# Performance work log

Measured on AMD Instinct MI355X. Metric: run time of the kernel, lower is better.

## Reference

```python
import jax, jax.numpy as jnp
import numpy as np
from jax import lax


def setup_inputs() -> dict:
    key = jax.random.key(0)
    k1, k2 = jax.random.split(key)
    B, T, D, O = 8, 8192, 512, 512
    x = jax.random.normal(k1, (B, T, D), dtype=jnp.float32)
    # Dense kernel over concat([h_t, state]) -> width 2*D
    W = jax.random.normal(k2, (2 * D, O), dtype=jnp.float32) * (1.0 / np.sqrt(2 * D))
    b = jnp.zeros((O,), dtype=jnp.float32)
    decay = jnp.float32(0.95)
    return {"x": x, "W": W, "b": b, "decay": decay}


def reference(x, W, b, decay):
    # x: [B, T, D]; W: [2D, O]; b: [O]; decay: scalar lambda
    B, T, D = x.shape
    lam = jnp.clip(decay, 0.5, 0.999)  # keras constraint on the decay weight
    h_avg = jnp.mean(x, axis=0)  # [T, D] batch-mean per timestep

    # EMA recurrence: s_t = lam * s_{t-1} + (1 - lam) * h_avg_t, s_{-1} = 0
    def step(s, a):
        s = lam * s + (1.0 - lam) * a
        return s, s

    _, states = lax.scan(step, jnp.zeros((D,), x.dtype), h_avg)  # [T, D]

    # proj(concat([h_t, s_t])) = h_t @ W_h + s_t @ W_s + b (fused, no concat materialized)
    W_h, W_s = W[:D], W[D:]
    out = jnp.einsum('btd,do->bto', x, W_h) + jnp.einsum('td,do->to', states, W_s)[None] + b
    return out  # [B, T, O]
```

## Files before the change

### kernel.cpp

```cpp
#include <hip/hip_runtime.h>
#include <hip/hip_bf16.h>
#include <stdint.h>

#define T_DIM 8192
#define B_DIM 8
#define D_DIM 512
#define O_DIM 512

typedef __attribute__((ext_vector_type(4))) float f32x4;
typedef __attribute__((ext_vector_type(8))) short short8;
typedef __attribute__((ext_vector_type(4))) unsigned short us4;
typedef __attribute__((ext_vector_type(4))) uint32_t u32x4;

__device__ __forceinline__ unsigned short f2bf(float f) {
  union { float f; uint32_t u; } v; v.f = f;
  uint32_t u = v.u + 0x7FFFu + ((v.u >> 16) & 1u);
  return (unsigned short)(u >> 16);
}

__device__ __forceinline__ uint32_t cvtpk(float a, float b) {
  uint32_t r;
  asm("v_cvt_pk_bf16_f32 %0, %1, %2" : "=v"(r) : "v"(a), "v"(b));
  return r;
}

__device__ __forceinline__ void gload_lds16(const void* g, void* l) {
  __builtin_amdgcn_global_load_lds(
      (const __attribute__((address_space(1))) void*)g,
      (__attribute__((address_space(3))) void*)l, 16, 0, 0);
}

__device__ __forceinline__ float clip_lam(const float* decay) {
  return fminf(fmaxf(decay[0], 0.5f), 0.999f);
}

__global__ void mean_kernel(const float* __restrict__ x, float* __restrict__ havg) {
  int idx = blockIdx.x * 256 + threadIdx.x;
  const f32x4* x4 = (const f32x4*)x;
  const size_t stride = (size_t)T_DIM * D_DIM / 4;
  f32x4 v[8];
#pragma unroll
  for (int b = 0; b < B_DIM; ++b) v[b] = x4[(size_t)b * stride + idx];
  f32x4 s = ((v[0] + v[1]) + (v[2] + v[3])) + ((v[4] + v[5]) + (v[6] + v[7]));
  s *= 0.125f;
  ((f32x4*)havg)[idx] = s;
}

__global__ void wconv_kernel(const float* __restrict__ W, unsigned short* __restrict__ Wt) {
  __shared__ float tile[64][65];
  int bk = blockIdx.x >> 3;
  int bn = blockIdx.x & 7;
  int tr = threadIdx.x >> 4;
  int tc = threadIdx.x & 15;
#pragma unroll
  for (int i = 0; i < 4; ++i) {
    int row = i * 16 + tr;
    f32x4 v = *(const f32x4*)&W[(size_t)(bk * 64 + row) * O_DIM + bn * 64 + tc * 4];
#pragma unroll
    for (int j = 0; j < 4; ++j) tile[row][tc * 4 + j] = v[j];
  }
  __syncthreads();
#pragma unroll
  for (int i = 0; i < 4; ++i) {
    int nl = i * 16 + tr;
    us4 o;
#pragma unroll
    for (int j = 0; j < 4; ++j) o[j] = f2bf(tile[tc * 4 + j][nl]);
    int kg = bk * 64 + tc * 4;
    int h = kg >> 9;
    int k = kg & 511;
    *(us4*)&Wt[(size_t)h * (512 * 512) + (size_t)(bn * 64 + nl) * 512 + k] = o;
  }
}

#define CHUNK 128
#define NCHUNK (T_DIM / CHUNK)

__global__ void scanA_kernel(float* __restrict__ havg, const float* __restrict__ decay) {
  int chunk = blockIdx.x >> 1;
  int d = ((blockIdx.x & 1) << 8) + threadIdx.x;
  float lam = clip_lam(decay);
  float om = 1.0f - lam;
  size_t base = (size_t)chunk * CHUNK * D_DIM + d;
  float cur[16], nxt[16];
#pragma unroll
  for (int i = 0; i < 16; ++i) cur[i] = havg[base + (size_t)i * D_DIM];
  float s = 0.f;
  for (int blk = 0; blk < 8; ++blk) {
    if (blk < 7) {
#pragma unroll
      for (int i = 0; i < 16; ++i)
        nxt[i] = havg[base + (size_t)((blk + 1) * 16 + i) * D_DIM];
    }
#pragma unroll
    for (int i = 0; i < 16; ++i) {
      s = lam * s + om * cur[i];
      havg[base + (size_t)(blk * 16 + i) * D_DIM] = s;
    }
#pragma unroll
    for (int i = 0; i < 16; ++i) cur[i] = nxt[i];
  }
}

__global__ void scanB_kernel(const float* __restrict__ havg, const float* __restrict__ decay,
                             float* __restrict__ carry) {
  int d = blockIdx.x * 256 + threadIdx.x;
  float lam = clip_lam(decay);
  float l2 = lam * lam;
  float l4 = l2 * l2;
  float l8 = l4 * l4;
  float l16 = l8 * l8;
  float l32 = l16 * l16;
  float l64 = l32 * l32;
  float l128 = l64 * l64;
  float e[NCHUNK];
#pragma unroll
  for (int c = 0; c < NCHUNK; ++c)
    e[c] = havg[((size_t)c * CHUNK + CHUNK - 1) * D_DIM + d];
  float s = 0.f;
#pragma unroll
  for (int c = 0; c < NCHUNK; ++c) {
    s = l128 * s + e[c];
    carry[c * D_DIM + d] = s;
  }
}

__global__ void scanC_kernel(const float* __restrict__ havg, const float* __restrict__ carry,
                             const float* __restrict__ decay, unsigned short* __restrict__ st) {
  int idx = blockIdx.x * 256 + threadIdx.x;
  int t = idx >> 7;
  int d4 = idx & 127;
  int c = t >> 7;
  int k = t & 127;
  float lam = clip_lam(decay);
  float w = exp2f((float)(k + 1) * __log2f(lam));
  f32x4 p = ((const f32x4*)havg)[idx];
  f32x4 cin = {0.f, 0.f, 0.f, 0.f};
  if (c > 0) cin = ((const f32x4*)carry)[(size_t)(c - 1) * 128 + d4];
  us4 o;
#pragma unroll
  for (int j = 0; j < 4; ++j) o[j] = f2bf(p[j] + w * cin[j]);
  ((us4*)st)[idx] = o;
}

__global__ __launch_bounds__(256, 4)
void gemm128bf(const unsigned short* __restrict__ A, const unsigned short* __restrict__ Bt,
               const float* __restrict__ extra, float* __restrict__ C) {
  __shared__ __align__(16) char smem[2][16384];

  int nwg = gridDim.x;
  int bid = blockIdx.x;
  int swz = (bid & 7) * (nwg >> 3) + (bid >> 3);
  int tm = swz >> 2, tn = swz & 3;
  int brow = tm << 7, bcol = tn << 7;

  int tid = threadIdx.x;
  int wave = tid >> 6, lane = tid & 63;
  int wr = (wave >> 1) << 6, wc = (wave & 1) << 6;
  const int lr = lane & 15, lkb = lane >> 4;

  const int soct = ((lane & 3) ^ ((lane >> 3) & 3)) << 3;
  const int pm = (lr >> 1) & 3;

  const size_t a_base = (size_t)(brow + (wave << 4) + (lane >> 2)) * 512 + soct;
  const size_t b_base = (size_t)(bcol + (wave << 4) + (lane >> 2)) * 512 + soct;

  f32x4 acc[4][4];
#pragma unroll
  for (int m = 0; m < 4; ++m)
#pragma unroll
    for (int n = 0; n < 4; ++n) acc[m][n] = (f32x4){0.f, 0.f, 0.f, 0.f};

#define STAGE(buf, kt_)                                                        \
  {                                                                            \
    int k0_ = (kt_) << 5;                                                      \
    _Pragma("unroll")                                                          \
    for (int it = 0; it < 2; ++it)                                             \
      gload_lds16(A + a_base + (size_t)(it << 15) + k0_,                       \
                  &smem[buf][(((it << 2) + wave) << 10)]);                     \
    _Pragma("unroll")                                                          \
    for (int it = 0; it < 2; ++it)                                             \
      gload_lds16(Bt + b_base + (size_t)(it << 15) + k0_,                      \
                  &smem[buf][8192 + (((it << 2) + wave) << 10)]);              \
  }

  STAGE(0, 0);

#pragma unroll 2
  for (int kt = 0; kt < 16; ++kt) {
    const int cur = kt & 1;
    if (kt < 15) {
      STAGE(cur ^ 1, kt + 1);
      asm volatile("s_waitcnt vmcnt(4)" ::: "memory");
    } else {
      asm volatile("s_waitcnt vmcnt(0)" ::: "memory");
    }
    __builtin_amdgcn_s_barrier();
    __builtin_amdgcn_sched_barrier(0);

    const unsigned short* As = (const unsigned short*)&smem[cur][0];
    const unsigned short* Bs = (const unsigned short*)&smem[cur][8192];
    short8 af[4], bfr[4];
#pragma unroll
    for (int m = 0; m < 4; ++m)
      af[m] = *(const short8*)(As + (size_t)(wr + (m << 4) + lr) * 32 + ((lkb ^ pm) << 3));
#pragma unroll
    for (int n = 0; n < 4; ++n)
      bfr[n] = *(const short8*)(Bs + (size_t)(wc + (n << 4) + lr) * 32 + ((lkb ^ pm) << 3));

#pragma unroll
    for (int m = 0; m < 4; ++m)
#pragma unroll
      for (int n = 0; n < 4; ++n)
        acc[m][n] = __builtin_amdgcn_mfma_f32_16x16x32_bf16(af[m], bfr[n], acc[m][n], 0, 0, 0);

    __builtin_amdgcn_sched_barrier(0);
    __builtin_amdgcn_s_barrier();
  }
#undef STAGE

  float* tp = (float*)&smem[0][0] + (size_t)wave * 2048;
#pragma unroll
  for (int m = 0; m < 4; ++m) {
#pragma unroll
    for (int n = 0; n < 4; ++n)
#pragma unroll
      for (int j = 0; j < 4; ++j)
        tp[((lkb << 2) + j) * 68 + (n << 4) + lr] = acc[m][n][j];
    __syncthreads();
#pragma unroll
    for (int p = 0; p < 4; ++p) {
      int rl = (p << 2) + (lane >> 4);
      int c0 = (lane & 15) << 2;
      f32x4 v = *(const f32x4*)(tp + rl * 68 + c0);
      int row = brow + wr + (m << 4) + rl;
      int col = bcol + wc + c0;
      f32x4 e = *(const f32x4*)&extra[col];
      v += e;
      *(f32x4*)&C[(size_t)row * O_DIM + col] = v;
    }
    __syncthreads();
  }
}

__global__ __launch_bounds__(256, 4)
void gemm128xf(const float* __restrict__ X, const unsigned short* __restrict__ Bt,
               const float* __restrict__ extra, float* __restrict__ C) {
  __shared__ __align__(16) char smem[2][16384];

  int nwg = gridDim.x;
  int bid = blockIdx.x;
  int swz = (bid & 7) * (nwg >> 3) + (bid >> 3);
  int tm = swz >> 2, tn = swz & 3;
  int brow = tm << 7, bcol = tn << 7;

  int tid = threadIdx.x;
  int wave = tid >> 6, lane = tid & 63;
  int wr = (wave >> 1) << 6, wc = (wave & 1) << 6;
  const int lr = lane & 15, lkb = lane >> 4;
  const int pm = (lr >> 1) & 3;

  const int arow = tid >> 1, ahalf = tid & 1;
  const float* agp = X + (size_t)(brow + arow) * 512 + (ahalf << 4);
  const int aperm = (arow >> 1) & 3;
  const int aw0 = arow * 64 + (((ahalf << 1) ^ aperm) << 4);
  const int aw1 = aw0 ^ 16;

  const int soct = ((lane & 3) ^ ((lane >> 3) & 3)) << 3;
  const size_t b_base = (size_t)(bcol + (wave << 4) + (lane >> 2)) * 512 + soct;

  f32x4 acc[4][4];
#pragma unroll
  for (int m = 0; m < 4; ++m)
#pragma unroll
    for (int n = 0; n < 4; ++n) acc[m][n] = (f32x4){0.f, 0.f, 0.f, 0.f};

  f32x4 a0, a1, a2, a3;
#define ALOAD(kt_)                                                             \
  {                                                                            \
    const float* p_ = agp + ((kt_) << 5);                                      \
    a0 = *(const f32x4*)p_;       a1 = *(const f32x4*)(p_ + 4);                \
    a2 = *(const f32x4*)(p_ + 8); a3 = *(const f32x4*)(p_ + 12);               \
  }
#define BSTAGE(buf, kt_)                                                       \
  {                                                                            \
    int k0_ = (kt_) << 5;                                                      \
    _Pragma("unroll")                                                          \
    for (int it = 0; it < 2; ++it)                                             \
      gload_lds16(Bt + b_base + (size_t)(it << 15) + k0_,                      \
                  &smem[buf][8192 + (((it << 2) + wave) << 10)]);              \
  }
#define AWRITE(buf)                                                            \
  {                                                                            \
    u32x4 w0_ = {cvtpk(a0[0], a0[1]), cvtpk(a0[2], a0[3]),                     \
                 cvtpk(a1[0], a1[1]), cvtpk(a1[2], a1[3])};                    \
    u32x4 w1_ = {cvtpk(a2[0], a2[1]), cvtpk(a2[2], a2[3]),                     \
                 cvtpk(a3[0], a3[1]), cvtpk(a3[2], a3[3])};                    \
    *(u32x4*)&smem[buf][aw0] = w0_;                                            \
    *(u32x4*)&smem[buf][aw1] = w1_;                                            \
  }

  ALOAD(0); BSTAGE(0, 0);
  AWRITE(0);
  __syncthreads();

#pragma unroll 2
  for (int kt = 0; kt < 16; ++kt) {
    const int cur = kt & 1;
    if (kt < 15) { ALOAD(kt + 1); BSTAGE(cur ^ 1, kt + 1); }
    __builtin_amdgcn_sched_barrier(0);

    const unsigned short* As = (const unsigned short*)&smem[cur][0];
    const unsigned short* Bs = (const unsigned short*)&smem[cur][8192];
    short8 af[4], bfr[4];
#pragma unroll
    for (int m = 0; m < 4; ++m)
      af[m] = *(const short8*)(As + (size_t)(wr + (m << 4) + lr) * 32 + ((lkb ^ pm) << 3));
#pragma unroll
    for (int n = 0; n < 4; ++n)
      bfr[n] = *(const short8*)(Bs + (size_t)(wc + (n << 4) + lr) * 32 + ((lkb ^ pm) << 3));

#pragma unroll
    for (int m = 0; m < 4; ++m)
#pragma unroll
      for (int n = 0; n < 4; ++n)
        acc[m][n] = __builtin_amdgcn_mfma_f32_16x16x32_bf16(af[m], bfr[n], acc[m][n], 0, 0, 0);

    if (kt < 15) AWRITE(cur ^ 1);
    __syncthreads();
  }
#undef ALOAD
#undef BSTAGE
#undef AWRITE

  float* tp = (float*)&smem[0][0] + (size_t)wave * 2048;
#pragma unroll
  for (int m = 0; m < 4; ++m) {
#pragma unroll
    for (int n = 0; n < 4; ++n)
#pragma unroll
      for (int j = 0; j < 4; ++j)
        tp[((lkb << 2) + j) * 68 + (n << 4) + lr] = acc[m][n][j];
    __syncthreads();
#pragma unroll
    for (int p = 0; p < 4; ++p) {
      int rl = (p << 2) + (lane >> 4);
      int c0 = (lane & 15) << 2;
      f32x4 v = *(const f32x4*)(tp + rl * 68 + c0);
      int row = brow + wr + (m << 4) + rl;
      int col = bcol + wc + c0;
      f32x4 e = *(const f32x4*)&extra[(size_t)(row & (T_DIM - 1)) * O_DIM + col];
      v += e;
      *(f32x4*)&C[(size_t)row * O_DIM + col] = v;
    }
    __syncthreads();
  }
}

extern "C" void kernel_launch(void* const* d_in, const int* in_sizes, int n_in,
                              void* d_out, int out_size, void* d_ws, size_t ws_size,
                              hipStream_t stream) {
  (void)in_sizes; (void)n_in; (void)out_size; (void)ws_size;
  const float* x     = (const float*)d_in[0];
  const float* W     = (const float*)d_in[1];
  const float* bias  = (const float*)d_in[2];
  const float* decay = (const float*)d_in[3];
  float* out = (float*)d_out;

  char* ws = (char*)d_ws;
  size_t off = 0;
  float*          havg  = (float*)(ws + off);          off += 16777216;
  unsigned short* st    = (unsigned short*)(ws + off); off += 8388608;
  unsigned short* Wt    = (unsigned short*)(ws + off); off += 1048576;
  float*          sbar  = (float*)(ws + off);          off += 16777216;
  float*          carry = (float*)(ws + off);          off += 131072;

  mean_kernel<<<T_DIM * D_DIM / 4 / 256, 256, 0, stream>>>(x, havg);
  wconv_kernel<<<128, 256, 0, stream>>>(W, Wt);
  scanA_kernel<<<NCHUNK * 2, 256, 0, stream>>>(havg, decay);
  scanB_kernel<<<2, 256, 0, stream>>>(havg, decay, carry);
  scanC_kernel<<<T_DIM * D_DIM / 4 / 256, 256, 0, stream>>>(havg, carry, decay, st);
  gemm128bf<<<(T_DIM / 128) * 4, 256, 0, stream>>>(st, Wt + 512 * 512, bias, sbar);
  gemm128xf<<<(B_DIM * T_DIM / 128) * 4, 256, 0, stream>>>(x, Wt, sbar, out);
}
```

Before: 129.8 us.

## Load GEMM operands directly from global into MFMA registers, bypassing LDS staging

New measurement: 239.0 us. 84.1% more time.

```diff
diff --git a/kernel.cpp b/kernel.cpp
--- a/kernel.cpp
+++ b/kernel.cpp
@@ -243,10 +243,10 @@
   }
 }
 
-__global__ __launch_bounds__(256, 4)
-void gemm128xf(const float* __restrict__ X, const unsigned short* __restrict__ Bt,
-               const float* __restrict__ extra, float* __restrict__ C) {
-  __shared__ __align__(16) char smem[2][16384];
+__global__ __launch_bounds__(256, 3)
+void gemm_direct(const float* __restrict__ X, const unsigned short* __restrict__ Wt,
+                 const float* __restrict__ sbar, float* __restrict__ C) {
+  __shared__ __align__(16) char smem[32768];
 
   int nwg = gridDim.x;
   int bid = blockIdx.x;
@@ -258,16 +258,15 @@
   int wave = tid >> 6, lane = tid & 63;
   int wr = (wave >> 1) << 6, wc = (wave & 1) << 6;
   const int lr = lane & 15, lkb = lane >> 4;
-  const int pm = (lr >> 1) & 3;
-
-  const int arow = tid >> 1, ahalf = tid & 1;
-  const float* agp = X + (size_t)(brow + arow) * 512 + (ahalf << 4);
-  const int aperm = (arow >> 1) & 3;
-  const int aw0 = arow * 64 + (((ahalf << 1) ^ aperm) << 4);
-  const int aw1 = aw0 ^ 16;
-
-  const int soct = ((lane & 3) ^ ((lane >> 3) & 3)) << 3;
-  const size_t b_base = (size_t)(bcol + (wave << 4) + (lane >> 2)) * 512 + soct;
+
+  const float* ax[4];
+  const unsigned short* bw[4];
+#pragma unroll
+  for (int m = 0; m < 4; ++m)
+    ax[m] = X + (size_t)(brow + wr + (m << 4) + lr) * 512 + (lkb << 3);
+#pragma unroll
+  for (int n = 0; n < 4; ++n)
+    bw[n] = Wt + (size_t)(bcol + wc + (n << 4) + lr) * 512 + (lkb << 3);
 
   f32x4 acc[4][4];
 #pragma unroll
@@ -275,65 +274,48 @@
 #pragma unroll
     for (int n = 0; n < 4; ++n) acc[m][n] = (f32x4){0.f, 0.f, 0.f, 0.f};
 
-  f32x4 a0, a1, a2, a3;
-#define ALOAD(kt_)                                                             \
-  {                                                                            \
-    const float* p_ = agp + ((kt_) << 5);                                      \
-    a0 = *(const f32x4*)p_;       a1 = *(const f32x4*)(p_ + 4);                \
-    a2 = *(const f32x4*)(p_ + 8); a3 = *(const f32x4*)(p_ + 12);               \
-  }
-#define BSTAGE(buf, kt_)                                                       \
-  {                                                                            \
-    int k0_ = (kt_) << 5;                                                      \
-    _Pragma("unroll")                                                          \
-    for (int it = 0; it < 2; ++it)                                             \
-      gload_lds16(Bt + b_base + (size_t)(it << 15) + k0_,                      \
-                  &smem[buf][8192 + (((it << 2) + wave) << 10)]);              \
-  }
-#define AWRITE(buf)                                                            \
-  {                                                                            \
-    u32x4 w0_ = {cvtpk(a0[0], a0[1]), cvtpk(a0[2], a0[3]),                     \
-                 cvtpk(a1[0], a1[1]), cvtpk(a1[2], a1[3])};                    \
-    u32x4 w1_ = {cvtpk(a2[0], a2[1]), cvtpk(a2[2], a2[3]),                     \
-                 cvtpk(a3[0], a3[1]), cvtpk(a3[2], a3[3])};                    \
-    *(u32x4*)&smem[buf][aw0] = w0_;                                            \
-    *(u32x4*)&smem[buf][aw1] = w1_;                                            \
-  }
-
-  ALOAD(0); BSTAGE(0, 0);
-  AWRITE(0);
-  __syncthreads();
-
-#pragma unroll 2
+  f32x4 a0[4], a1[4];
+  short8 bl[4];
+#pragma unroll
+  for (int m = 0; m < 4; ++m) {
+    a0[m] = *(const f32x4*)(ax[m]);
+    a1[m] = *(const f32x4*)(ax[m] + 4);
+  }
+#pragma unroll
+  for (int n = 0; n < 4; ++n) bl[n] = *(const short8*)(bw[n]);
+
   for (int kt = 0; kt < 16; ++kt) {
-    const int cur = kt & 1;
-    if (kt < 15) { ALOAD(kt + 1); BSTAGE(cur ^ 1, kt + 1); }
-    __builtin_amdgcn_sched_barrier(0);
-
-    const unsigned short* As = (const unsigned short*)&smem[cur][0];
-    const unsigned short* Bs = (const unsigned short*)&smem[cur][8192];
-    short8 af[4], bfr[4];
+    short8 af[4];
+#pragma unroll
+    for (int m = 0; m < 4; ++m) {
+      union { short8 s; u32x4 u; } t;
+      t.u = (u32x4){cvtpk(a0[m][0], a0[m][1]), cvtpk(a0[m][2], a0[m][3]),
+                    cvtpk(a1[m][0], a1[m][1]), cvtpk(a1[m][2], a1[m][3])};
+      af[m] = t.s;
+    }
+    short8 bf[4];
+#pragma unroll
+    for (int n = 0; n < 4; ++n) bf[n] = bl[n];
+
+    if (kt < 15) {
+      int off = (kt + 1) << 5;
+#pragma unroll
+      for (int m = 0; m < 4; ++m) {
+        a0[m] = *(const f32x4*)(ax[m] + off);
+        a1[m] = *(const f32x4*)(ax[m] + off + 4);
+      }
+#pragma unroll
+      for (int n = 0; n < 4; ++n) bl[n] = *(const short8*)(bw[n] + off);
+    }
+
 #pragma unroll
     for (int m = 0; m < 4; ++m)
-      af[m] = *(const short8*)(As + (size_t)(wr + (m << 4) + lr) * 32 + ((lkb ^ pm) << 3));
-#pragma unroll
-    for (int n = 0; n < 4; ++n)
-      bfr[n] = *(const short8*)(Bs + (size_t)(wc + (n << 4) + lr) * 32 + ((lkb ^ pm) << 3));
-
-#pragma unroll
-    for (int m = 0; m < 4; ++m)
 #pragma unroll
       for (int n = 0; n < 4; ++n)
-        acc[m][n] = __builtin_amdgcn_mfma_f32_16x16x32_bf16(af[m], bfr[n], acc[m][n], 0, 0, 0);
-
-    if (kt < 15) AWRITE(cur ^ 1);
-    __syncthreads();
-  }
-#undef ALOAD
-#undef BSTAGE
-#undef AWRITE
-
-  float* tp = (float*)&smem[0][0] + (size_t)wave * 2048;
+        acc[m][n] = __builtin_amdgcn_mfma_f32_16x16x32_bf16(af[m], bf[n], acc[m][n], 0, 0, 0);
+  }
+
+  float* tp = (float*)smem + (size_t)wave * 2048;
 #pragma unroll
   for (int m = 0; m < 4; ++m) {
 #pragma unroll
@@ -349,7 +331,7 @@
       f32x4 v = *(const f32x4*)(tp + rl * 68 + c0);
       int row = brow + wr + (m << 4) + rl;
       int col = bcol + wc + c0;
-      f32x4 e = *(const f32x4*)&extra[(size_t)(row & (T_DIM - 1)) * O_DIM + col];
+      f32x4 e = *(const f32x4*)&sbar[(size_t)(row & (T_DIM - 1)) * O_DIM + col];
       v += e;
       *(f32x4*)&C[(size_t)row * O_DIM + col] = v;
     }
@@ -381,5 +363,5 @@
   scanB_kernel<<<2, 256, 0, stream>>>(havg, decay, carry);
   scanC_kernel<<<T_DIM * D_DIM / 4 / 256, 256, 0, stream>>>(havg, carry, decay, st);
   gemm128bf<<<(T_DIM / 128) * 4, 256, 0, stream>>>(st, Wt + 512 * 512, bias, sbar);
-  gemm128xf<<<(B_DIM * T_DIM / 128) * 4, 256, 0, stream>>>(x, Wt, sbar, out);
-}
+  gemm_direct<<<(B_DIM * T_DIM / 128) * 4, 256, 0, stream>>>(x, Wt, sbar, out);
+}
```
